# Optimization experiments

Hardware: AMD Instinct MI355X
Metric: run time of the kernel (lower is better)

The kernel has to match this reference:

```python
import jax, jax.numpy as jnp
import numpy as np

D_MODEL = 2048
N_HEADS = 16
HEAD_DIM = 128          # d_model * expand_factor // n_heads
HP = N_HEADS // 2       # head pairs
EPS = 1e-6
LAYER_DEPTH = 6
LAMBDA_INIT = 0.8 - 0.6 * float(np.exp(-0.3 * LAYER_DEPTH))
ROPE_BASE = 10000.0


def rmsnorm(x, eps=EPS):
    return x * jax.lax.rsqrt(jnp.mean(x * x, axis=-1, keepdims=True) + eps)


def rope_tables(T, dim, base=ROPE_BASE):
    inv_freq = 1.0 / base ** (jnp.arange(0, dim, 2, dtype=jnp.float32) / dim)
    t = jnp.arange(T, dtype=jnp.float32)
    freqs = jnp.outer(t, inv_freq)               # (T, dim/2)
    return jnp.cos(freqs), jnp.sin(freqs)


def apply_rotary(x, cos, sin):
    # x: (B,T,H,dim); cos/sin: (T, dim/2)
    d = x.shape[-1] // 2
    x1, x2 = x[..., :d], x[..., d:]
    c = cos[None, :, None, :]
    s = sin[None, :, None, :]
    return jnp.concatenate([x1 * c + x2 * s, -x1 * s + x2 * c], axis=-1)


def setup_inputs() -> dict:
    key = jax.random.key(0)
    ks = jax.random.split(key, 7)
    B, T = 2, 2048
    qkv_out = N_HEADS * HEAD_DIM + 2 * N_HEADS * HEAD_DIM  # 6144
    return {
        "hidden_states": jax.random.normal(ks[0], (B, T, D_MODEL), jnp.float32),
        "W_qkv": jax.random.normal(ks[1], (D_MODEL, qkv_out), jnp.float32) * (D_MODEL ** -0.5),
        "lambda_q1": jax.random.normal(ks[2], (HP, HEAD_DIM // 2), jnp.float32) * 0.1,
        "lambda_k1": jax.random.normal(ks[3], (HP, HEAD_DIM // 2), jnp.float32) * 0.1,
        "lambda_q2": jax.random.normal(ks[4], (HP, HEAD_DIM // 2), jnp.float32) * 0.1,
        "lambda_k2": jax.random.normal(ks[5], (HP, HEAD_DIM // 2), jnp.float32) * 0.1,
        "W_g": jax.random.normal(ks[6], (D_MODEL, D_MODEL), jnp.float32) * (D_MODEL ** -0.5),
    }


def _causal_attn(q, k, v, scale):
    # q,k: (B,T,Hp,hd), v: (B,T,Hp,2*hd) -> (B,T,Hp,2*hd)
    T = q.shape[1]
    scores = jnp.einsum("bqhd,bkhd->bhqk", q, k) * scale
    mask = jnp.tril(jnp.ones((T, T), dtype=bool))
    scores = jnp.where(mask[None, None], scores, -jnp.inf)
    attn = jax.nn.softmax(scores, axis=-1)
    return jnp.einsum("bhqk,bkhd->bqhd", attn, v)


def reference(hidden_states, W_qkv, lambda_q1, lambda_k1, lambda_q2, lambda_k2, W_g):
    x = hidden_states
    B, T, _ = x.shape
    qkv = x @ W_qkv                                     # (B,T,6144)
    qkv = qkv.reshape(B, T, N_HEADS, 3 * HEAD_DIM)      # n_rep=1: per kv head [q|k|v]
    q = qkv[..., :HEAD_DIM]
    k = qkv[..., HEAD_DIM:2 * HEAD_DIM]
    v = qkv[..., 2 * HEAD_DIM:]
    v = v.reshape(B, T, HP, 2 * HEAD_DIM)               # pair value heads
    # qk RMSNorm (no affine), then RoPE
    q = rmsnorm(q)
    k = rmsnorm(k)
    cos, sin = rope_tables(T, HEAD_DIM)
    q = apply_rotary(q, cos, sin)
    k = apply_rotary(k, cos, sin)
    # split even/odd heads
    q1, q2 = q[:, :, 0::2], q[:, :, 1::2]
    k1, k2 = k[:, :, 0::2], k[:, :, 1::2]
    scale = HEAD_DIM ** -0.5
    y1 = _causal_attn(q1, k1, v, scale)
    y2 = _causal_attn(q2, k2, v, scale)
    lam1 = jnp.exp(jnp.sum(lambda_q1 * lambda_k1, axis=-1))
    lam2 = jnp.exp(jnp.sum(lambda_q2 * lambda_k2, axis=-1))
    lam = (lam1 - lam2 + LAMBDA_INIT)[None, None, :, None]  # (1,1,Hp,1)
    y = y1 - lam * y2                                    # (B,T,Hp,2*hd)
    # elementwise silu gate
    g = jax.nn.silu(x @ W_g).reshape(B, T, HP, 2 * HEAD_DIM)
    y = y * g
    # group RMSNorm over 2*head_dim (no affine), then DIFF rescale
    y = rmsnorm(y) * (1.0 - LAMBDA_INIT)
    return y.reshape(B, T, D_MODEL)
```

## Files before the change

### kernel.cpp

```cpp
#include <hip/hip_runtime.h>
#include <stdint.h>

#define TSEQ 2048
#define DMODEL 2048
#define NQKV 6144
#define NTOT 8192

static constexpr float LAM_INIT = 0.7008206670670481f;
static constexpr float QK_SCALE = 0.08838834764831845f;
static constexpr float NEG_BIG = -1e30f;

typedef float f32x4 __attribute__((ext_vector_type(4)));
typedef short s16x8 __attribute__((ext_vector_type(8)));

__device__ __forceinline__ unsigned short f2bf(float f) {
  unsigned u = __builtin_bit_cast(unsigned, f);
  u += 0x7fffu + ((u >> 16) & 1u);
  return (unsigned short)(u >> 16);
}
__device__ __forceinline__ float bf2f(unsigned short h) {
  unsigned u = ((unsigned)h) << 16;
  return __builtin_bit_cast(float, u);
}
__device__ __forceinline__ unsigned pk2(float a, float b) {
  return (unsigned)f2bf(a) | ((unsigned)f2bf(b) << 16);
}

__device__ __forceinline__ void mfma_bf16(f32x4& d, s16x8 a, s16x8 b) {
  asm("v_mfma_f32_16x16x32_bf16 %0, %1, %2, %0" : "+v"(d) : "v"(a), "v"(b));
}

__device__ __forceinline__ void gld_lds16(const void* g, void* l) {
  __builtin_amdgcn_global_load_lds(
      (const __attribute__((address_space(1))) unsigned int*)g,
      (__attribute__((address_space(3))) unsigned int*)l, 16, 0, 0);
}

__global__ void k_cvt(const float* __restrict__ in, unsigned short* __restrict__ o, int n) {
  const int i = (blockIdx.x * 256 + threadIdx.x) * 8;
  if (i >= n) return;
  float4 a = *(const float4*)(in + i);
  float4 b = *(const float4*)(in + i + 4);
  uint4 u;
  u.x = pk2(a.x, a.y); u.y = pk2(a.z, a.w);
  u.z = pk2(b.x, b.y); u.w = pk2(b.z, b.w);
  *(uint4*)(o + i) = u;
}

__global__ void k_rope(float* __restrict__ ct, float* __restrict__ st) {
  const int id = blockIdx.x * 256 + threadIdx.x;
  const int t = id >> 6, j = id & 63;
  const float inv = powf(10000.f, -(float)j * (1.f / 64.f));
  const float f = (float)t * inv;
  ct[id] = cosf(f);
  st[id] = sinf(f);
}

__global__ void k_trans(const float* __restrict__ W, unsigned short* __restrict__ wt,
                        int N, int rowoff) {
  __shared__ __align__(16) unsigned short tl[64][72];
  const int tid = threadIdx.x;
  const int n0 = blockIdx.x * 64, k0 = blockIdx.y * 64;
#pragma unroll
  for (int i = 0; i < 4; ++i) {
    const int idx = tid + i * 256;
    const int r = idx >> 4, c4 = idx & 15;
    float4 v = *(const float4*)(W + (size_t)(k0 + r) * N + n0 + c4 * 4);
    tl[c4 * 4 + 0][r] = f2bf(v.x);
    tl[c4 * 4 + 1][r] = f2bf(v.y);
    tl[c4 * 4 + 2][r] = f2bf(v.z);
    tl[c4 * 4 + 3][r] = f2bf(v.w);
  }
  __syncthreads();
#pragma unroll
  for (int i = 0; i < 2; ++i) {
    const int idx = tid + i * 256;
    const int rn = idx >> 3, c8 = idx & 7;
    uint4 vv = *(const uint4*)(&tl[rn][c8 * 8]);
    *(uint4*)(wt + (size_t)(rowoff + n0 + rn) * 2048 + k0 + c8 * 8) = vv;
  }
}

__global__ __launch_bounds__(256, 2) void k_gemm(
    const unsigned short* __restrict__ A, const unsigned short* __restrict__ B,
    unsigned short* __restrict__ C) {
  __shared__ __align__(16) unsigned short As[128 * 64];
  __shared__ __align__(16) unsigned short Bs[128 * 64];
  const int tid = threadIdx.x;
  const int l = tid & 63;
  const int ll = l & 15, lg = l >> 4;
  const int w = tid >> 6;
  const int wm = (w >> 1) * 64, wn = (w & 1) * 64;
  const int m0 = blockIdx.y * 128;
  const int n0 = blockIdx.x * 128;

  f32x4 acc[4][4];
#pragma unroll
  for (int i = 0; i < 4; ++i)
#pragma unroll
    for (int j = 0; j < 4; ++j) acc[i][j] = (f32x4){0.f, 0.f, 0.f, 0.f};

  for (int kt = 0; kt < 32; ++kt) {
    const int k0 = kt * 64;
    __syncthreads();
#pragma unroll
    for (int i = 0; i < 4; ++i) {
      const int s = tid + i * 256;
      const int row = s >> 3;
      const int col = ((s & 7) ^ (row & 7)) << 3;
      gld_lds16(A + (size_t)(m0 + row) * 2048 + k0 + col, &As[s * 8]);
      gld_lds16(B + (size_t)(n0 + row) * 2048 + k0 + col, &Bs[s * 8]);
    }
    __syncthreads();
#pragma unroll
    for (int kc = 0; kc < 2; ++kc) {
      s16x8 af[4], bfv[4];
#pragma unroll
      for (int mf = 0; mf < 4; ++mf) {
        const int r = wm + mf * 16 + ll;
        af[mf] = *(const s16x8*)((const char*)As + r * 128 +
                                 ((kc * 64 + lg * 16) ^ ((r & 7) << 4)));
      }
#pragma unroll
      for (int nf = 0; nf < 4; ++nf) {
        const int r = wn + nf * 16 + ll;
        bfv[nf] = *(const s16x8*)((const char*)Bs + r * 128 +
                                  ((kc * 64 + lg * 16) ^ ((r & 7) << 4)));
      }
#pragma unroll
      for (int mf = 0; mf < 4; ++mf)
#pragma unroll
        for (int nf = 0; nf < 4; ++nf) mfma_bf16(acc[mf][nf], af[mf], bfv[nf]);
    }
  }
  const bool gate = (n0 >= NQKV);
#pragma unroll
  for (int mf = 0; mf < 4; ++mf)
#pragma unroll
    for (int nf = 0; nf < 4; ++nf)
#pragma unroll
      for (int r = 0; r < 4; ++r) {
        const int row = m0 + wm + mf * 16 + lg * 4 + r;
        const int col = n0 + wn + nf * 16 + ll;
        float v = acc[mf][nf][r];
        if (gate) v = v / (1.f + __expf(-v));
        C[(size_t)row * NTOT + col] = f2bf(v);
      }
}

__global__ void k_post(const unsigned short* __restrict__ cc,
                       const float* __restrict__ ctab, const float* __restrict__ stab,
                       unsigned short* __restrict__ qb, unsigned short* __restrict__ kb,
                       unsigned short* __restrict__ vtb) {
  __shared__ __align__(16) unsigned short lv[128][72];
  const int tid = threadIdx.x;
  const int t0 = blockIdx.x * 64;
  const int H = blockIdx.y;
  const int b = blockIdx.z;
  const int row = tid >> 2, c = tid & 3;
  const int t = t0 + row;
  const int sd = H & 1, sh = H >> 1;
  const size_t qkbase = ((((size_t)sd * 2 + b) * 8 + sh) * TSEQ) * 128;
  const size_t ccrow = (size_t)(b * TSEQ + t) * NTOT + (size_t)H * 384;

#pragma unroll
  for (int part = 0; part < 2; ++part) {
    const unsigned short* src = cc + ccrow + part * 128 + c * 32;
    float x[32];
#pragma unroll
    for (int j = 0; j < 4; ++j) {
      uint4 v = *(const uint4*)(src + j * 8);
      x[j * 8 + 0] = bf2f((unsigned short)(v.x & 0xffff));
      x[j * 8 + 1] = bf2f((unsigned short)(v.x >> 16));
      x[j * 8 + 2] = bf2f((unsigned short)(v.y & 0xffff));
      x[j * 8 + 3] = bf2f((unsigned short)(v.y >> 16));
      x[j * 8 + 4] = bf2f((unsigned short)(v.z & 0xffff));
      x[j * 8 + 5] = bf2f((unsigned short)(v.z >> 16));
      x[j * 8 + 6] = bf2f((unsigned short)(v.w & 0xffff));
      x[j * 8 + 7] = bf2f((unsigned short)(v.w >> 16));
    }
    float ssq = 0.f;
#pragma unroll
    for (int i = 0; i < 32; ++i) ssq += x[i] * x[i];
    ssq += __shfl_xor(ssq, 1);
    ssq += __shfl_xor(ssq, 2);
    const float rms = rsqrtf(ssq * (1.f / 128.f) + 1e-6f);
#pragma unroll
    for (int i = 0; i < 32; ++i) x[i] *= rms;
    float px[32];
#pragma unroll
    for (int i = 0; i < 32; ++i) px[i] = __shfl_xor(x[i], 2);
    const int jb = (c & 1) * 32;
    const float sgn = (c < 2) ? 1.f : -1.f;
    float ov[32];
#pragma unroll
    for (int i = 0; i < 32; ++i) {
      const float cs = ctab[t * 64 + jb + i];
      const float sn = stab[t * 64 + jb + i];
      ov[i] = x[i] * cs + sgn * px[i] * sn;
    }
    unsigned short* dst = (part == 0 ? qb : kb) + qkbase + (size_t)t * 128 + c * 32;
#pragma unroll
    for (int j = 0; j < 4; ++j) {
      uint4 u;
      u.x = pk2(ov[j * 8 + 0], ov[j * 8 + 1]);
      u.y = pk2(ov[j * 8 + 2], ov[j * 8 + 3]);
      u.z = pk2(ov[j * 8 + 4], ov[j * 8 + 5]);
      u.w = pk2(ov[j * 8 + 6], ov[j * 8 + 7]);
      *(uint4*)(dst + j * 8) = u;
    }
  }

  {
    const unsigned short* src = cc + ccrow + 256 + c * 32;
#pragma unroll
    for (int j = 0; j < 4; ++j) {
      uint4 v = *(const uint4*)(src + j * 8);
      const int base = c * 32 + j * 8;
      lv[base + 0][row] = (unsigned short)(v.x & 0xffff);
      lv[base + 1][row] = (unsigned short)(v.x >> 16);
      lv[base + 2][row] = (unsigned short)(v.y & 0xffff);
      lv[base + 3][row] = (unsigned short)(v.y >> 16);
      lv[base + 4][row] = (unsigned short)(v.z & 0xffff);
      lv[base + 5][row] = (unsigned short)(v.z >> 16);
      lv[base + 6][row] = (unsigned short)(v.w & 0xffff);
      lv[base + 7][row] = (unsigned short)(v.w >> 16);
    }
  }
  __syncthreads();
#pragma unroll
  for (int i = 0; i < 4; ++i) {
    const int sl = tid + i * 256;
    const int dv = sl >> 3, c8 = sl & 7;
    uint4 vv = *(const uint4*)(&lv[dv][c8 * 8]);
    const size_t off = (((size_t)b * 8 + sh) * 256 + sd * 128 + dv) * TSEQ + t0 + c8 * 8;
    *(uint4*)(vtb + off) = vv;
  }
}

__device__ __forceinline__ void attn_stage(const unsigned short* kg, const unsigned short* vg,
                                           unsigned short* Kd, unsigned short* Vd, int tid) {
#pragma unroll
  for (int i = 0; i < 4; ++i) {
    const int sl = tid + i * 256;
    const int row = sl >> 4;
    const int p = sl & 15;
    const int col = (((p & 8) | ((p & 7) ^ (row & 7)))) << 3;
    gld_lds16(kg + (size_t)row * 128 + col, Kd + sl * 8);
  }
#pragma unroll
  for (int i = 0; i < 8; ++i) {
    const int sl = tid + i * 256;
    const int row = sl >> 3;
    const int col = ((sl & 7) ^ (row & 7)) << 3;
    gld_lds16(vg + (size_t)row * TSEQ + col, Vd + sl * 8);
  }
}

__global__ __launch_bounds__(256, 1) void k_attn(
    const unsigned short* __restrict__ qb, const unsigned short* __restrict__ kb,
    const unsigned short* __restrict__ vtb, unsigned short* __restrict__ ys) {
  __shared__ __align__(16) unsigned short Ks[2][64 * 128];
  __shared__ __align__(16) unsigned short Vts[2][256 * 64];
  __shared__ __align__(16) unsigned short Ps[128 * 72];
  __shared__ float scs[128];
  __shared__ float lbuf[128];

  const int tid = threadIdx.x;
  const int l = tid & 63;
  const int ll = l & 15, lg = l >> 4;
  const int w = tid >> 6;
  const int qt = blockIdx.x;
  const int sh = blockIdx.y;
  const int b = blockIdx.z >> 1;
  const int s = blockIdx.z & 1;

  const size_t qkbase = ((((size_t)s * 2 + b) * 8 + sh) * TSEQ) * 128;
  const size_t vtbase = (((size_t)b * 8 + sh) * 256) * TSEQ;

  s16x8 qfr[2][4];
#pragma unroll
  for (int qf = 0; qf < 2; ++qf)
#pragma unroll
    for (int dc = 0; dc < 4; ++dc) {
      const int row = qt * 128 + w * 32 + qf * 16 + ll;
      qfr[qf][dc] = *(const s16x8*)(qb + qkbase + (size_t)row * 128 + dc * 32 + lg * 8);
    }

  float m_[2][4], ls_[2][4];
#pragma unroll
  for (int qf = 0; qf < 2; ++qf)
#pragma unroll
    for (int r = 0; r < 4; ++r) { m_[qf][r] = NEG_BIG; ls_[qf][r] = 0.f; }

  f32x4 acc[4][8];
#pragma unroll
  for (int i = 0; i < 4; ++i)
#pragma unroll
    for (int j = 0; j < 8; ++j) acc[i][j] = (f32x4){0.f, 0.f, 0.f, 0.f};

  const int qrow0 = (w >> 1) * 64;
  const int dv0 = (w & 1) * 128;
  const int nkt = 2 * qt + 2;

  attn_stage(kb + qkbase + (size_t)0 * 128, vtb + vtbase + 0, Ks[0], Vts[0], tid);
  __syncthreads();

  for (int kt = 0; kt < nkt; ++kt) {
    const int cur = kt & 1;
    if (kt + 1 < nkt)
      attn_stage(kb + qkbase + (size_t)((kt + 1) * 64) * 128, vtb + vtbase + (kt + 1) * 64,
                 Ks[cur ^ 1], Vts[cur ^ 1], tid);

    f32x4 sacc[2][4];
#pragma unroll
    for (int qf = 0; qf < 2; ++qf)
#pragma unroll
      for (int kvf = 0; kvf < 4; ++kvf) sacc[qf][kvf] = (f32x4){0.f, 0.f, 0.f, 0.f};
#pragma unroll
    for (int dc = 0; dc < 4; ++dc) {
#pragma unroll
      for (int kvf = 0; kvf < 4; ++kvf) {
        const int r = kvf * 16 + ll;
        s16x8 kf = *(const s16x8*)((const char*)Ks[cur] + r * 256 +
                                   ((dc * 64 + lg * 16) ^ ((r & 7) << 4)));
        mfma_bf16(sacc[0][kvf], qfr[0][dc], kf);
        mfma_bf16(sacc[1][kvf], qfr[1][dc], kf);
      }
    }
    const bool mask = (kt >= 2 * qt);
#pragma unroll
    for (int qf = 0; qf < 2; ++qf) {
      float sv[4][4];
#pragma unroll
      for (int kvf = 0; kvf < 4; ++kvf)
#pragma unroll
        for (int r = 0; r < 4; ++r) {
          float xv = sacc[qf][kvf][r] * QK_SCALE;
          if (mask) {
            const int kvg = kt * 64 + kvf * 16 + ll;
            const int qg = qt * 128 + w * 32 + qf * 16 + lg * 4 + r;
            if (kvg > qg) xv = NEG_BIG;
          }
          sv[kvf][r] = xv;
        }
#pragma unroll
      for (int r = 0; r < 4; ++r) {
        float mx = fmaxf(fmaxf(sv[0][r], sv[1][r]), fmaxf(sv[2][r], sv[3][r]));
        mx = fmaxf(mx, __shfl_xor(mx, 1));
        mx = fmaxf(mx, __shfl_xor(mx, 2));
        mx = fmaxf(mx, __shfl_xor(mx, 4));
        mx = fmaxf(mx, __shfl_xor(mx, 8));
        const float mnew = fmaxf(m_[qf][r], mx);
        const float scr = __expf(m_[qf][r] - mnew);
        m_[qf][r] = mnew;
        float rs = 0.f;
#pragma unroll
        for (int kvf = 0; kvf < 4; ++kvf) {
          const float p = __expf(sv[kvf][r] - mnew);
          sv[kvf][r] = p;
          rs += p;
        }
        rs += __shfl_xor(rs, 1);
        rs += __shfl_xor(rs, 2);
        rs += __shfl_xor(rs, 4);
        rs += __shfl_xor(rs, 8);
        ls_[qf][r] = ls_[qf][r] * scr + rs;
        const int prow = w * 32 + qf * 16 + lg * 4 + r;
        if (ll == 0) scs[prow] = scr;
#pragma unroll
        for (int kvf = 0; kvf < 4; ++kvf)
          Ps[prow * 72 + kvf * 16 + ll] = f2bf(sv[kvf][r]);
      }
    }
    __syncthreads();

    float scv[4][4];
#pragma unroll
    for (int qf = 0; qf < 4; ++qf)
#pragma unroll
      for (int r = 0; r < 4; ++r) scv[qf][r] = scs[qrow0 + qf * 16 + lg * 4 + r];
#pragma unroll
    for (int qf = 0; qf < 4; ++qf)
#pragma unroll
      for (int dvf = 0; dvf < 8; ++dvf) {
        f32x4 t = acc[qf][dvf];
        t[0] *= scv[qf][0]; t[1] *= scv[qf][1]; t[2] *= scv[qf][2]; t[3] *= scv[qf][3];
        acc[qf][dvf] = t;
      }
#pragma unroll
    for (int kc = 0; kc < 2; ++kc) {
      s16x8 pa[4];
#pragma unroll
      for (int qf = 0; qf < 4; ++qf)
        pa[qf] = *(const s16x8*)((const char*)Ps + (qrow0 + qf * 16 + ll) * 144 +
                                 kc * 64 + lg * 16);
#pragma unroll
      for (int dvf = 0; dvf < 8; ++dvf) {
        const int r = dv0 + dvf * 16 + ll;
        s16x8 vb = *(const s16x8*)((const char*)Vts[cur] + r * 128 +
                                   ((kc * 64 + lg * 16) ^ ((r & 7) << 4)));
#pragma unroll
        for (int qf = 0; qf < 4; ++qf) mfma_bf16(acc[qf][dvf], pa[qf], vb);
      }
    }
    __syncthreads();
  }

  if (ll == 0) {
#pragma unroll
    for (int qf = 0; qf < 2; ++qf)
#pragma unroll
      for (int r = 0; r < 4; ++r) lbuf[w * 32 + qf * 16 + lg * 4 + r] = ls_[qf][r];
  }
  __syncthreads();
  const size_t ybase = ((((size_t)s * 2 + b) * 8 + sh) * TSEQ) * 256;
#pragma unroll
  for (int qf = 0; qf < 4; ++qf) {
    float li[4];
#pragma unroll
    for (int r = 0; r < 4; ++r) li[r] = 1.f / lbuf[qrow0 + qf * 16 + lg * 4 + r];
#pragma unroll
    for (int dvf = 0; dvf < 8; ++dvf)
#pragma unroll
      for (int r = 0; r < 4; ++r) {
        const int row = qt * 128 + qrow0 + qf * 16 + lg * 4 + r;
        const int col = dv0 + dvf * 16 + ll;
        ys[ybase + (size_t)row * 256 + col] = f2bf(acc[qf][dvf][r] * li[r]);
      }
  }
}

__global__ void k_final(const unsigned short* __restrict__ ys,
                        const unsigned short* __restrict__ cc,
                        const float* __restrict__ lq1, const float* __restrict__ lk1,
                        const float* __restrict__ lq2, const float* __restrict__ lk2,
                        float* __restrict__ out) {
  const int tid = threadIdx.x;
  const int row = tid >> 2, c = tid & 3;
  const int t = blockIdx.x * 64 + row;
  const int sh = blockIdx.y;
  const int b = blockIdx.z;

  float d1 = 0.f, d2 = 0.f;
  for (int j = 0; j < 64; ++j) {
    d1 += lq1[sh * 64 + j] * lk1[sh * 64 + j];
    d2 += lq2[sh * 64 + j] * lk2[sh * 64 + j];
  }
  const float lam = __expf(d1) - __expf(d2) + LAM_INIT;

  const size_t y1o = ((((size_t)0 * 2 + b) * 8 + sh) * TSEQ + t) * 256 + c * 64;
  const size_t y2o = ((((size_t)1 * 2 + b) * 8 + sh) * TSEQ + t) * 256 + c * 64;
  const size_t go = (size_t)(b * TSEQ + t) * NTOT + NQKV + sh * 256 + c * 64;

  float y[64];
#define UNPK(r0, r1, aa, dd, gg)                                                   \
  r0 = (bf2f((unsigned short)((aa) & 0xffff)) - lam * bf2f((unsigned short)((dd) & 0xffff))) * \
       bf2f((unsigned short)((gg) & 0xffff));                                      \
  r1 = (bf2f((unsigned short)((aa) >> 16)) - lam * bf2f((unsigned short)((dd) >> 16))) *       \
       bf2f((unsigned short)((gg) >> 16));
#pragma unroll
  for (int j = 0; j < 8; ++j) {
    uint4 a = *(const uint4*)(ys + y1o + j * 8);
    uint4 d = *(const uint4*)(ys + y2o + j * 8);
    uint4 g = *(const uint4*)(cc + go + j * 8);
    UNPK(y[j * 8 + 0], y[j * 8 + 1], a.x, d.x, g.x)
    UNPK(y[j * 8 + 2], y[j * 8 + 3], a.y, d.y, g.y)
    UNPK(y[j * 8 + 4], y[j * 8 + 5], a.z, d.z, g.z)
    UNPK(y[j * 8 + 6], y[j * 8 + 7], a.w, d.w, g.w)
  }
#undef UNPK
  float ssq = 0.f;
#pragma unroll
  for (int i = 0; i < 64; ++i) ssq += y[i] * y[i];
  ssq += __shfl_xor(ssq, 1);
  ssq += __shfl_xor(ssq, 2);
  const float sc = rsqrtf(ssq * (1.f / 256.f) + 1e-6f) * (1.f - LAM_INIT);
  float* op = out + (size_t)(b * TSEQ + t) * DMODEL + sh * 256 + c * 64;
#pragma unroll
  for (int j = 0; j < 16; ++j) {
    float4 v = {y[j * 4] * sc, y[j * 4 + 1] * sc, y[j * 4 + 2] * sc, y[j * 4 + 3] * sc};
    *(float4*)(op + j * 4) = v;
  }
}

extern "C" void kernel_launch(void* const* d_in, const int* in_sizes, int n_in,
                              void* d_out, int out_size, void* d_ws, size_t ws_size,
                              hipStream_t stream) {
  (void)in_sizes; (void)n_in; (void)out_size; (void)ws_size;
  const float* x = (const float*)d_in[0];
  const float* wqkv = (const float*)d_in[1];
  const float* lq1 = (const float*)d_in[2];
  const float* lk1 = (const float*)d_in[3];
  const float* lq2 = (const float*)d_in[4];
  const float* lk2 = (const float*)d_in[5];
  const float* wg = (const float*)d_in[6];
  float* out = (float*)d_out;
  char* ws = (char*)d_ws;

  unsigned short* xb = (unsigned short*)(ws);
  unsigned short* wt = (unsigned short*)(ws + (size_t)16777216);
  unsigned short* cc = (unsigned short*)(ws + (size_t)50331648);
  unsigned short* ysb = (unsigned short*)(ws + (size_t)117440512);
  float* ctab = (float*)(ws + (size_t)150994944);
  float* stab = (float*)(ws + (size_t)151519232);
  unsigned short* qbf = (unsigned short*)(ws);
  unsigned short* kbf = (unsigned short*)(ws + (size_t)16777216);
  unsigned short* vtb = (unsigned short*)(ws + (size_t)33554432);

  hipLaunchKernelGGL(k_cvt, dim3(4096), dim3(256), 0, stream, x, xb, 8388608);
  hipLaunchKernelGGL(k_rope, dim3(512), dim3(256), 0, stream, ctab, stab);
  hipLaunchKernelGGL(k_trans, dim3(96, 32), dim3(256), 0, stream, wqkv, wt, 6144, 0);
  hipLaunchKernelGGL(k_trans, dim3(32, 32), dim3(256), 0, stream, wg, wt, 2048, 6144);
  hipLaunchKernelGGL(k_gemm, dim3(64, 32), dim3(256), 0, stream, xb, wt, cc);
  hipLaunchKernelGGL(k_post, dim3(32, 16, 2), dim3(256), 0, stream, cc, ctab, stab, qbf, kbf, vtb);
  hipLaunchKernelGGL(k_attn, dim3(16, 8, 4), dim3(256), 0, stream, qbf, kbf, vtb, ysb);
  hipLaunchKernelGGL(k_final, dim3(32, 8, 2), dim3(256), 0, stream, ysb, cc, lq1, lk1, lq2, lk2, out);
}
```

Baseline: 715.3 us.

## Load V fragments directly from global into registers, drop V LDS staging

The attention kernel no longer stages V tiles through double-buffered shared memory. Each wave now loads its V fragments straight from global memory into registers at the start of every key tile. This cuts LDS usage enough to allow two blocks per CU (launch bounds changed to 2). The grid is flattened to 1D and query tiles are paired in reverse order so long and short causal blocks interleave for load balance. The risks are register pressure from 16 extra vector registers per lane under the tighter bound, and global load latency that is no longer hidden by the prefetch pipeline.

```diff
diff --git a/kernel.cpp b/kernel.cpp
--- a/kernel.cpp
+++ b/kernel.cpp
@@ -238,8 +238,7 @@
   }
 }
 
-__device__ __forceinline__ void attn_stage(const unsigned short* kg, const unsigned short* vg,
-                                           unsigned short* Kd, unsigned short* Vd, int tid) {
+__device__ __forceinline__ void stage_k(const unsigned short* kg, unsigned short* Kd, int tid) {
 #pragma unroll
   for (int i = 0; i < 4; ++i) {
     const int sl = tid + i * 256;
@@ -248,20 +247,12 @@
     const int col = (((p & 8) | ((p & 7) ^ (row & 7)))) << 3;
     gld_lds16(kg + (size_t)row * 128 + col, Kd + sl * 8);
   }
-#pragma unroll
-  for (int i = 0; i < 8; ++i) {
-    const int sl = tid + i * 256;
-    const int row = sl >> 3;
-    const int col = ((sl & 7) ^ (row & 7)) << 3;
-    gld_lds16(vg + (size_t)row * TSEQ + col, Vd + sl * 8);
-  }
-}
-
-__global__ __launch_bounds__(256, 1) void k_attn(
+}
+
+__global__ __launch_bounds__(256, 2) void k_attn(
     const unsigned short* __restrict__ qb, const unsigned short* __restrict__ kb,
     const unsigned short* __restrict__ vtb, unsigned short* __restrict__ ys) {
   __shared__ __align__(16) unsigned short Ks[2][64 * 128];
-  __shared__ __align__(16) unsigned short Vts[2][256 * 64];
   __shared__ __align__(16) unsigned short Ps[128 * 72];
   __shared__ float scs[128];
   __shared__ float lbuf[128];
@@ -270,10 +261,17 @@
   const int l = tid & 63;
   const int ll = l & 15, lg = l >> 4;
   const int w = tid >> 6;
-  const int qt = blockIdx.x;
-  const int sh = blockIdx.y;
-  const int b = blockIdx.z >> 1;
-  const int s = blockIdx.z & 1;
+
+  const int i = blockIdx.x;
+  const int u = i & 255;
+  const int h = i >> 8;
+  const int p4 = u & 15;
+  const int qt = h ? (15 - p4) : p4;
+  const int sh = (u >> 4) & 7;
+  const int z = u >> 7;
+  const int bs = z * 2 + h;
+  const int b = bs & 1;
+  const int s = bs >> 1;
 
   const size_t qkbase = ((((size_t)s * 2 + b) * 8 + sh) * TSEQ) * 128;
   const size_t vtbase = (((size_t)b * 8 + sh) * 256) * TSEQ;
@@ -295,22 +293,29 @@
 
   f32x4 acc[4][8];
 #pragma unroll
-  for (int i = 0; i < 4; ++i)
-#pragma unroll
-    for (int j = 0; j < 8; ++j) acc[i][j] = (f32x4){0.f, 0.f, 0.f, 0.f};
+  for (int a = 0; a < 4; ++a)
+#pragma unroll
+    for (int j = 0; j < 8; ++j) acc[a][j] = (f32x4){0.f, 0.f, 0.f, 0.f};
 
   const int qrow0 = (w >> 1) * 64;
   const int dv0 = (w & 1) * 128;
   const int nkt = 2 * qt + 2;
 
-  attn_stage(kb + qkbase + (size_t)0 * 128, vtb + vtbase + 0, Ks[0], Vts[0], tid);
+  stage_k(kb + qkbase, Ks[0], tid);
   __syncthreads();
 
   for (int kt = 0; kt < nkt; ++kt) {
     const int cur = kt & 1;
+    s16x8 vb[2][8];
+#pragma unroll
+    for (int kc = 0; kc < 2; ++kc)
+#pragma unroll
+      for (int dvf = 0; dvf < 8; ++dvf)
+        vb[kc][dvf] = *(const s16x8*)(vtb + vtbase +
+                                      (size_t)(dv0 + dvf * 16 + ll) * TSEQ +
+                                      kt * 64 + kc * 32 + lg * 8);
     if (kt + 1 < nkt)
-      attn_stage(kb + qkbase + (size_t)((kt + 1) * 64) * 128, vtb + vtbase + (kt + 1) * 64,
-                 Ks[cur ^ 1], Vts[cur ^ 1], tid);
+      stage_k(kb + qkbase + (size_t)(kt + 1) * 64 * 128, Ks[cur ^ 1], tid);
 
     f32x4 sacc[2][4];
 #pragma unroll
@@ -396,13 +401,9 @@
         pa[qf] = *(const s16x8*)((const char*)Ps + (qrow0 + qf * 16 + ll) * 144 +
                                  kc * 64 + lg * 16);
 #pragma unroll
-      for (int dvf = 0; dvf < 8; ++dvf) {
-        const int r = dv0 + dvf * 16 + ll;
-        s16x8 vb = *(const s16x8*)((const char*)Vts[cur] + r * 128 +
-                                   ((kc * 64 + lg * 16) ^ ((r & 7) << 4)));
-#pragma unroll
-        for (int qf = 0; qf < 4; ++qf) mfma_bf16(acc[qf][dvf], pa[qf], vb);
-      }
+      for (int dvf = 0; dvf < 8; ++dvf)
+#pragma unroll
+        for (int qf = 0; qf < 4; ++qf) mfma_bf16(acc[qf][dvf], pa[qf], vb[kc][dvf]);
     }
     __syncthreads();
   }
@@ -514,6 +515,6 @@
   hipLaunchKernelGGL(k_trans, dim3(32, 32), dim3(256), 0, stream, wg, wt, 2048, 6144);
   hipLaunchKernelGGL(k_gemm, dim3(64, 32), dim3(256), 0, stream, xb, wt, cc);
   hipLaunchKernelGGL(k_post, dim3(32, 16, 2), dim3(256), 0, stream, cc, ctab, stab, qbf, kbf, vtb);
-  hipLaunchKernelGGL(k_attn, dim3(16, 8, 4), dim3(256), 0, stream, qbf, kbf, vtb, ysb);
+  hipLaunchKernelGGL(k_attn, dim3(512), dim3(256), 0, stream, qbf, kbf, vtb, ysb);
   hipLaunchKernelGGL(k_final, dim3(32, 8, 2), dim3(256), 0, stream, ysb, cc, lq1, lk1, lq2, lk2, out);
 }
```

Result: slower. 762.3 us (+6.6%).
